# Performance work log

Hardware: AMD Instinct MI355X
Metric: run time of the kernel (lower is better)

Reference implementation:

```python
import jax, jax.numpy as jnp
import numpy as np
from jax import lax

KS = 11          # kernel_size
SIGMA = 1.5
MAX_VAL = 1.0
C1 = (0.01 * MAX_VAL) ** 2
C2 = (0.03 * MAX_VAL) ** 2
EPS = 1e-12
PAD = KS // 2    # use_padding=True -> reflect pad


def _gaussian_kernel3d():
    ax = jnp.arange(KS, dtype=jnp.float32) - (KS - 1) / 2.0
    g = jnp.exp(-(ax[:, None, None] ** 2 + ax[None, :, None] ** 2 + ax[None, None, :] ** 2)
                / (2.0 * SIGMA ** 2))
    return g / g.sum()  # (KS, KS, KS)


def setup_inputs() -> dict:
    key = jax.random.key(0)
    k1, k2 = jax.random.split(key)
    shape = (2, 1, 160, 160, 160)
    source = jax.random.uniform(k1, shape, dtype=jnp.float32)
    reference_vol = jax.random.uniform(k2, shape, dtype=jnp.float32)
    return {"source": source, "reference": reference_vol}


def reference(source, reference):
    B, C, H, W, D = source.shape
    # reflect pad spatial dims (torch 'reflect' == numpy 'reflect')
    pad_cfg = ((0, 0), (0, 0), (PAD, PAD), (PAD, PAD), (PAD, PAD))
    src = jnp.pad(source, pad_cfg, mode="reflect")
    ref = jnp.pad(reference, pad_cfg, mode="reflect")

    # fuse the 5 depthwise convolutions into one grouped conv over stacked channels
    stacked = jnp.concatenate([src, ref, src * src, ref * ref, src * ref], axis=1)  # (B,5C,...)
    kern = _gaussian_kernel3d()[None, None]                      # (1,1,KS,KS,KS)
    kern = jnp.tile(kern, (5 * C, 1, 1, 1, 1))                   # (5C,1,KS,KS,KS)
    out = lax.conv_general_dilated(
        stacked, kern, window_strides=(1, 1, 1), padding="VALID",
        feature_group_count=5 * C,
        dimension_numbers=("NCDHW", "OIDHW", "NCDHW"))           # (B,5C,H,W,D)

    mu1 = out[:, 0 * C:1 * C]
    mu2 = out[:, 1 * C:2 * C]
    m11 = out[:, 2 * C:3 * C]
    m22 = out[:, 3 * C:4 * C]
    m12 = out[:, 4 * C:5 * C]

    mu1_sq = mu1 * mu1
    mu2_sq = mu2 * mu2
    mu1_mu2 = mu1 * mu2
    sigma1_sq = m11 - mu1_sq
    sigma2_sq = m22 - mu2_sq
    sigma12 = m12 - mu1_mu2

    numerator = (2.0 * mu1_mu2 + C1) * (2.0 * sigma12 + C2)
    denominator = (mu1_sq + mu2_sq + C1) * (sigma1_sq + sigma2_sq + C2)
    ssim = numerator / (denominator + EPS)
    return 1.0 - ssim.mean()
```

## Files before the change

kernel.cpp:

```cpp
#include <hip/hip_runtime.h>
#include <math.h>

#define HH 160
#define WW 160
#define DD 160
#define VOL (HH*WW*DD)
#define KS 11
#define PAD 5
#define NBATCH 2
#define NTOT (NBATCH*VOL)
#define WCH 32
#define HCH 32

struct Wts { float w[KS]; };

__device__ __forceinline__ int mirror(int i, int n) {
    if (i < 0) i = -i;
    if (i >= n) i = 2*n - 2 - i;
    return i;
}

__global__ void init_out(float* out) {
    if (threadIdx.x == 0 && blockIdx.x == 0) out[0] = 1.0f;
}

__global__ __launch_bounds__(256) void k1(const float* __restrict__ src,
                                          const float* __restrict__ ref,
                                          float* __restrict__ B, Wts wts) {
    const int colsBlocks = HH * DD / 256;
    int colblk = blockIdx.x % colsBlocks;
    int rest   = blockIdx.x / colsBlocks;
    int wch    = rest % (WW / WCH);
    int b      = rest / (WW / WCH);
    int col    = colblk * 256 + threadIdx.x;
    int h = col / DD, d = col % DD;
    const int w0 = wch * WCH;

    const float* sp = src + (size_t)b * VOL + (size_t)h * WW * DD;
    const float* rp = ref + (size_t)b * VOL + (size_t)h * WW * DD;
    float*       op = B   + (size_t)b * 5 * VOL + (size_t)h * WW * DD + d;

    int midx[KS];
#pragma unroll
    for (int k = 0; k < KS; ++k) midx[k] = mirror(d - PAD + k, DD);

    float acc[5][KS];
#pragma unroll
    for (int c = 0; c < 5; ++c)
#pragma unroll
        for (int s = 0; s < KS; ++s) acc[c][s] = 0.f;

    const int NSTEP = WCH + 2 * PAD;
    for (int tb = 0; tb < 44; tb += 11) {
#pragma unroll
        for (int ts = 0; ts < 11; ++ts) {
            int t = tb + ts;
            if (t < NSTEP) {
                int wm   = mirror(w0 - PAD + t, WW);
                int woff = wm * DD;
                float mu1 = 0.f, mu2 = 0.f, m11 = 0.f, m22 = 0.f, m12 = 0.f;
#pragma unroll
                for (int k = 0; k < KS; ++k) {
                    float s = sp[woff + midx[k]];
                    float r = rp[woff + midx[k]];
                    float wt = wts.w[k];
                    float p = wt * s, q = wt * r;
                    mu1 += p; mu2 += q;
                    m11 = fmaf(p, s, m11);
                    m22 = fmaf(q, r, m22);
                    m12 = fmaf(p, r, m12);
                }
                float v[5] = {mu1, mu2, m11, m22, m12};
#pragma unroll
                for (int m = 0; m < 11; ++m) {
                    int slot = (ts + m) % 11;
                    float wt = wts.w[10 - m];
#pragma unroll
                    for (int c = 0; c < 5; ++c)
                        acc[c][slot] = fmaf(wt, v[c], acc[c][slot]);
                }
                int o = w0 - 10 + t;
                if (t >= 10) {
#pragma unroll
                    for (int c = 0; c < 5; ++c)
                        op[(size_t)c * VOL + (size_t)o * DD] = acc[c][ts];
                }
#pragma unroll
                for (int c = 0; c < 5; ++c) acc[c][ts] = 0.f;
            }
        }
    }
}

__global__ __launch_bounds__(256) void k2(const float* __restrict__ B,
                                          float* __restrict__ out,
                                          Wts wts, float scale) {
    const int colsBlocks = WW * DD / 256;
    int colblk = blockIdx.x % colsBlocks;
    int rest   = blockIdx.x / colsBlocks;
    int hch    = rest % (HH / HCH);
    int b      = rest / (HH / HCH);
    int col    = colblk * 256 + threadIdx.x;
    const int h0 = hch * HCH;
    const float* p = B + (size_t)b * 5 * VOL + col;
    const size_t HS = (size_t)WW * DD;

    float acc[5][KS];
#pragma unroll
    for (int c = 0; c < 5; ++c)
#pragma unroll
        for (int s = 0; s < KS; ++s) acc[c][s] = 0.f;

    float ssum = 0.f;
    const int NSTEP = HCH + 2 * PAD;
    for (int tb = 0; tb < 44; tb += 11) {
#pragma unroll
        for (int ts = 0; ts < 11; ++ts) {
            int t = tb + ts;
            if (t < NSTEP) {
                int hm = mirror(h0 - PAD + t, HH);
                size_t off = (size_t)hm * HS;
                float v0 = p[off];
                float v1 = p[off + 1 * (size_t)VOL];
                float v2 = p[off + 2 * (size_t)VOL];
                float v3 = p[off + 3 * (size_t)VOL];
                float v4 = p[off + 4 * (size_t)VOL];
#pragma unroll
                for (int m = 0; m < 11; ++m) {
                    int slot = (ts + m) % 11;
                    float wt = wts.w[10 - m];
                    acc[0][slot] = fmaf(wt, v0, acc[0][slot]);
                    acc[1][slot] = fmaf(wt, v1, acc[1][slot]);
                    acc[2][slot] = fmaf(wt, v2, acc[2][slot]);
                    acc[3][slot] = fmaf(wt, v3, acc[3][slot]);
                    acc[4][slot] = fmaf(wt, v4, acc[4][slot]);
                }
                if (t >= 10) {
                    float mu1 = acc[0][ts], mu2 = acc[1][ts];
                    float m11 = acc[2][ts], m22 = acc[3][ts], m12 = acc[4][ts];
                    float mu1sq = mu1 * mu1, mu2sq = mu2 * mu2, mu12 = mu1 * mu2;
                    float s1 = m11 - mu1sq, s2 = m22 - mu2sq, s12 = m12 - mu12;
                    const float C1 = 1e-4f, C2 = 9e-4f;
                    float num = (2.f * mu12 + C1) * (2.f * s12 + C2);
                    float den = (mu1sq + mu2sq + C1) * (s1 + s2 + C2);
                    ssum += num / (den + 1e-12f);
                }
#pragma unroll
                for (int c = 0; c < 5; ++c) acc[c][ts] = 0.f;
            }
        }
    }

#pragma unroll
    for (int off = 32; off > 0; off >>= 1)
        ssum += __shfl_down(ssum, off, 64);
    __shared__ float lsum[4];
    int lane = threadIdx.x & 63, wid = threadIdx.x >> 6;
    if (lane == 0) lsum[wid] = ssum;
    __syncthreads();
    if (threadIdx.x == 0) {
        float s = lsum[0] + lsum[1] + lsum[2] + lsum[3];
        atomicAdd(out, -s * scale);
    }
}

__global__ void brute(const float* __restrict__ src, const float* __restrict__ ref,
                      float* __restrict__ out, Wts wts, float scale) {
    long gi = (long)blockIdx.x * blockDim.x + threadIdx.x;
    float ssim = 0.f;
    if (gi < NTOT) {
        int v = (int)(gi % VOL);
        int b = (int)(gi / VOL);
        int d = v % DD;
        int w = (v / DD) % WW;
        int h = v / (DD * WW);
        const float* sp = src + (long)b * VOL;
        const float* rp = ref + (long)b * VOL;
        float a0 = 0.f, a1 = 0.f, a2 = 0.f, a3 = 0.f, a4 = 0.f;
        for (int i = 0; i < KS; ++i) {
            int hm = mirror(h + i - PAD, HH);
            float wx = wts.w[i];
            for (int j = 0; j < KS; ++j) {
                int wm = mirror(w + j - PAD, WW);
                float wxy = wx * wts.w[j];
                const float* sr = sp + ((long)hm * WW + wm) * DD;
                const float* rr = rp + ((long)hm * WW + wm) * DD;
                for (int k = 0; k < KS; ++k) {
                    int dm = mirror(d + k - PAD, DD);
                    float wt = wxy * wts.w[k];
                    float s = sr[dm], r = rr[dm];
                    a0 += wt * s; a1 += wt * r; a2 += wt * s * s;
                    a3 += wt * r * r; a4 += wt * s * r;
                }
            }
        }
        float mu1sq = a0 * a0, mu2sq = a1 * a1, mu12 = a0 * a1;
        float s1 = a2 - mu1sq, s2 = a3 - mu2sq, s12 = a4 - mu12;
        const float C1 = 1e-4f, C2 = 9e-4f;
        float num = (2.f * mu12 + C1) * (2.f * s12 + C2);
        float den = (mu1sq + mu2sq + C1) * (s1 + s2 + C2);
        ssim = num / (den + 1e-12f);
    }
#pragma unroll
    for (int off = 32; off > 0; off >>= 1)
        ssim += __shfl_down(ssim, off, 64);
    __shared__ float lsum[4];
    int lane = threadIdx.x & 63, wid = threadIdx.x >> 6;
    if (lane == 0) lsum[wid] = ssim;
    __syncthreads();
    if (threadIdx.x == 0) {
        float s = lsum[0] + lsum[1] + lsum[2] + lsum[3];
        atomicAdd(out, -s * scale);
    }
}

extern "C" void kernel_launch(void* const* d_in, const int* in_sizes, int n_in,
                              void* d_out, int out_size, void* d_ws, size_t ws_size,
                              hipStream_t stream) {
    const float* src = (const float*)d_in[0];
    const float* ref = (const float*)d_in[1];
    float* out = (float*)d_out;

    Wts wts;
    {
        double g[KS], s = 0.0;
        for (int i = 0; i < KS; ++i) {
            double a = (double)i - (KS - 1) / 2.0;
            g[i] = exp(-(a * a) / (2.0 * 1.5 * 1.5));
            s += g[i];
        }
        for (int i = 0; i < KS; ++i) wts.w[i] = (float)(g[i] / s);
    }

    const float scale = 1.0f / (float)NTOT;
    const size_t need = (size_t)NBATCH * 5 * VOL * sizeof(float);

    init_out<<<1, 64, 0, stream>>>(out);

    if (ws_size >= need) {
        float* B = (float*)d_ws;
        const int g1 = NBATCH * (WW / WCH) * (HH * DD / 256);
        const int g2 = NBATCH * (HH / HCH) * (WW * DD / 256);
        k1<<<g1, 256, 0, stream>>>(src, ref, B, wts);
        k2<<<g2, 256, 0, stream>>>(B, out, wts, scale);
    } else {
        const int BLK = 256;
        const long g = (NTOT + BLK - 1) / BLK;
        brute<<<(int)g, BLK, 0, stream>>>(src, ref, out, wts, scale);
    }
}
```

Measured before the change: 213.5 us.

## Fuse separable SSIM passes into one tiled kernel using shared-memory W convolution

Replaces the two-kernel scheme, which wrote a five-channel intermediate volume to global memory and read it back, with a single kernel. Each block owns a 16x16 (W,D) tile and streams along H. Per H-plane it convolves along D from global memory into a double-buffered LDS tile (with W halo), convolves along W from LDS, then keeps a register ring over H. This removes the large intermediate global round trip. In exchange it adds a block barrier per plane and recomputes the D-pass on halo rows (26 of 16 W rows). Loads along D are now only 16-wide, and the single __syncthreads per plane with a two-deep buffer may race between the W-pass reading buffer t&1 and the writes to the same buffer at t+2.

```diff
diff --git a/kernel.cpp b/kernel.cpp
--- a/kernel.cpp
+++ b/kernel.cpp
@@ -9,8 +9,15 @@
 #define PAD 5
 #define NBATCH 2
 #define NTOT (NBATCH*VOL)
-#define WCH 32
-#define HCH 32
+
+#define WT 16
+#define DT 16
+#define HT 32
+#define WPN (WT + 2*PAD)
+#define NP  (WPN * DT)
+#define LROW (2*DT + 2)
+#define LPLANE (WPN * LROW)
+#define LBUF (3 * LPLANE)
 
 struct Wts { float w[KS]; };
 
@@ -24,25 +31,50 @@
     if (threadIdx.x == 0 && blockIdx.x == 0) out[0] = 1.0f;
 }
 
-__global__ __launch_bounds__(256) void k1(const float* __restrict__ src,
-                                          const float* __restrict__ ref,
-                                          float* __restrict__ B, Wts wts) {
-    const int colsBlocks = HH * DD / 256;
-    int colblk = blockIdx.x % colsBlocks;
-    int rest   = blockIdx.x / colsBlocks;
-    int wch    = rest % (WW / WCH);
-    int b      = rest / (WW / WCH);
-    int col    = colblk * 256 + threadIdx.x;
-    int h = col / DD, d = col % DD;
-    const int w0 = wch * WCH;
-
-    const float* sp = src + (size_t)b * VOL + (size_t)h * WW * DD;
-    const float* rp = ref + (size_t)b * VOL + (size_t)h * WW * DD;
-    float*       op = B   + (size_t)b * 5 * VOL + (size_t)h * WW * DD + d;
-
-    int midx[KS];
-#pragma unroll
-    for (int k = 0; k < KS; ++k) midx[k] = mirror(d - PAD + k, DD);
+__global__ __launch_bounds__(256) void fused(const float* __restrict__ src,
+                                             const float* __restrict__ ref,
+                                             float* __restrict__ out,
+                                             Wts wts, float scale) {
+    __shared__ float sd[2][LBUF];
+
+    const int bx  = blockIdx.x;
+    const int dt_ = bx % (DD/DT);
+    const int wt_ = (bx / (DD/DT)) % (WW/WT);
+    const int ht_ = (bx / ((DD/DT)*(WW/WT))) % (HH/HT);
+    const int b   = bx / ((DD/DT)*(WW/WT)*(HH/HT));
+    const int d0 = dt_*DT, w0 = wt_*WT, h0 = ht_*HT;
+
+    const int tid = threadIdx.x;
+    const float* __restrict__ sp = src + (size_t)b*VOL;
+    const float* __restrict__ rp = ref + (size_t)b*VOL;
+
+    int tap0[KS], tap1[KS];
+    int ws0, ws1;
+    {
+        int wp = tid / DT, dl = tid % DT;
+        int wm = mirror(w0 - PAD + wp, WW);
+        int da = d0 + dl;
+#pragma unroll
+        for (int k = 0; k < KS; ++k)
+            tap0[k] = wm*DD + mirror(da - PAD + k, DD);
+        ws0 = wp*LROW + 2*dl;
+    }
+    const int pi1 = tid + 256;
+    const bool act1 = (pi1 < NP);
+    {
+        int pi = act1 ? pi1 : tid;
+        int wp = pi / DT, dl = pi % DT;
+        int wm = mirror(w0 - PAD + wp, WW);
+        int da = d0 + dl;
+#pragma unroll
+        for (int k = 0; k < KS; ++k)
+            tap1[k] = wm*DD + mirror(da - PAD + k, DD);
+        ws1 = wp*LROW + 2*dl;
+    }
+
+    const int wl  = tid / DT;
+    const int dl2 = tid % DT;
+    const int rb  = wl*LROW + 2*dl2;
 
     float acc[5][KS];
 #pragma unroll
@@ -50,85 +82,70 @@
 #pragma unroll
         for (int s = 0; s < KS; ++s) acc[c][s] = 0.f;
 
-    const int NSTEP = WCH + 2 * PAD;
+    float ssum = 0.f;
+    const int NSTEP = HT + 2*PAD;
+
     for (int tb = 0; tb < 44; tb += 11) {
 #pragma unroll
         for (int ts = 0; ts < 11; ++ts) {
-            int t = tb + ts;
+            const int t = tb + ts;
             if (t < NSTEP) {
-                int wm   = mirror(w0 - PAD + t, WW);
-                int woff = wm * DD;
-                float mu1 = 0.f, mu2 = 0.f, m11 = 0.f, m22 = 0.f, m12 = 0.f;
+                const int hm = mirror(h0 - PAD + t, HH);
+                const float* __restrict__ sh = sp + (size_t)hm*(WW*DD);
+                const float* __restrict__ rh = rp + (size_t)hm*(WW*DD);
+                float* __restrict__ buf = sd[t & 1];
+
+                {
+                    float mu1=0.f, mu2=0.f, m11=0.f, m22=0.f, m12=0.f;
+#pragma unroll
+                    for (int k = 0; k < KS; ++k) {
+                        float s = sh[tap0[k]];
+                        float r = rh[tap0[k]];
+                        float wt = wts.w[k];
+                        float p = wt*s, q = wt*r;
+                        mu1 += p; mu2 += q;
+                        m11 = fmaf(p, s, m11);
+                        m22 = fmaf(q, r, m22);
+                        m12 = fmaf(p, r, m12);
+                    }
+                    buf[ws0]              = mu1; buf[ws0+1]            = mu2;
+                    buf[LPLANE + ws0]     = m11; buf[LPLANE + ws0+1]   = m22;
+                    buf[2*LPLANE + ws0]   = m12;
+                }
+                if (act1) {
+                    float mu1=0.f, mu2=0.f, m11=0.f, m22=0.f, m12=0.f;
+#pragma unroll
+                    for (int k = 0; k < KS; ++k) {
+                        float s = sh[tap1[k]];
+                        float r = rh[tap1[k]];
+                        float wt = wts.w[k];
+                        float p = wt*s, q = wt*r;
+                        mu1 += p; mu2 += q;
+                        m11 = fmaf(p, s, m11);
+                        m22 = fmaf(q, r, m22);
+                        m12 = fmaf(p, r, m12);
+                    }
+                    buf[ws1]              = mu1; buf[ws1+1]            = mu2;
+                    buf[LPLANE + ws1]     = m11; buf[LPLANE + ws1+1]   = m22;
+                    buf[2*LPLANE + ws1]   = m12;
+                }
+                __syncthreads();
+
+                float v0=0.f, v1=0.f, v2=0.f, v3=0.f, v4=0.f;
 #pragma unroll
                 for (int k = 0; k < KS; ++k) {
-                    float s = sp[woff + midx[k]];
-                    float r = rp[woff + midx[k]];
-                    float wt = wts.w[k];
-                    float p = wt * s, q = wt * r;
-                    mu1 += p; mu2 += q;
-                    m11 = fmaf(p, s, m11);
-                    m22 = fmaf(q, r, m22);
-                    m12 = fmaf(p, r, m12);
-                }
-                float v[5] = {mu1, mu2, m11, m22, m12};
+                    const int o = rb + k*LROW;
+                    const float wt = wts.w[k];
+                    v0 = fmaf(wt, buf[o],              v0);
+                    v1 = fmaf(wt, buf[o+1],            v1);
+                    v2 = fmaf(wt, buf[LPLANE + o],     v2);
+                    v3 = fmaf(wt, buf[LPLANE + o+1],   v3);
+                    v4 = fmaf(wt, buf[2*LPLANE + o],   v4);
+                }
 #pragma unroll
                 for (int m = 0; m < 11; ++m) {
-                    int slot = (ts + m) % 11;
-                    float wt = wts.w[10 - m];
-#pragma unroll
-                    for (int c = 0; c < 5; ++c)
-                        acc[c][slot] = fmaf(wt, v[c], acc[c][slot]);
-                }
-                int o = w0 - 10 + t;
-                if (t >= 10) {
-#pragma unroll
-                    for (int c = 0; c < 5; ++c)
-                        op[(size_t)c * VOL + (size_t)o * DD] = acc[c][ts];
-                }
-#pragma unroll
-                for (int c = 0; c < 5; ++c) acc[c][ts] = 0.f;
-            }
-        }
-    }
-}
-
-__global__ __launch_bounds__(256) void k2(const float* __restrict__ B,
-                                          float* __restrict__ out,
-                                          Wts wts, float scale) {
-    const int colsBlocks = WW * DD / 256;
-    int colblk = blockIdx.x % colsBlocks;
-    int rest   = blockIdx.x / colsBlocks;
-    int hch    = rest % (HH / HCH);
-    int b      = rest / (HH / HCH);
-    int col    = colblk * 256 + threadIdx.x;
-    const int h0 = hch * HCH;
-    const float* p = B + (size_t)b * 5 * VOL + col;
-    const size_t HS = (size_t)WW * DD;
-
-    float acc[5][KS];
-#pragma unroll
-    for (int c = 0; c < 5; ++c)
-#pragma unroll
-        for (int s = 0; s < KS; ++s) acc[c][s] = 0.f;
-
-    float ssum = 0.f;
-    const int NSTEP = HCH + 2 * PAD;
-    for (int tb = 0; tb < 44; tb += 11) {
-#pragma unroll
-        for (int ts = 0; ts < 11; ++ts) {
-            int t = tb + ts;
-            if (t < NSTEP) {
-                int hm = mirror(h0 - PAD + t, HH);
-                size_t off = (size_t)hm * HS;
-                float v0 = p[off];
-                float v1 = p[off + 1 * (size_t)VOL];
-                float v2 = p[off + 2 * (size_t)VOL];
-                float v3 = p[off + 3 * (size_t)VOL];
-                float v4 = p[off + 4 * (size_t)VOL];
-#pragma unroll
-                for (int m = 0; m < 11; ++m) {
-                    int slot = (ts + m) % 11;
-                    float wt = wts.w[10 - m];
+                    const int slot = (ts + m) % 11;
+                    const float wt = wts.w[10 - m];
                     acc[0][slot] = fmaf(wt, v0, acc[0][slot]);
                     acc[1][slot] = fmaf(wt, v1, acc[1][slot]);
                     acc[2][slot] = fmaf(wt, v2, acc[2][slot]);
@@ -138,10 +155,10 @@
                 if (t >= 10) {
                     float mu1 = acc[0][ts], mu2 = acc[1][ts];
                     float m11 = acc[2][ts], m22 = acc[3][ts], m12 = acc[4][ts];
-                    float mu1sq = mu1 * mu1, mu2sq = mu2 * mu2, mu12 = mu1 * mu2;
+                    float mu1sq = mu1*mu1, mu2sq = mu2*mu2, mu12 = mu1*mu2;
                     float s1 = m11 - mu1sq, s2 = m22 - mu2sq, s12 = m12 - mu12;
                     const float C1 = 1e-4f, C2 = 9e-4f;
-                    float num = (2.f * mu12 + C1) * (2.f * s12 + C2);
+                    float num = (2.f*mu12 + C1) * (2.f*s12 + C2);
                     float den = (mu1sq + mu2sq + C1) * (s1 + s2 + C2);
                     ssum += num / (den + 1e-12f);
                 }
@@ -155,63 +172,11 @@
     for (int off = 32; off > 0; off >>= 1)
         ssum += __shfl_down(ssum, off, 64);
     __shared__ float lsum[4];
-    int lane = threadIdx.x & 63, wid = threadIdx.x >> 6;
+    int lane = tid & 63, wid = tid >> 6;
     if (lane == 0) lsum[wid] = ssum;
     __syncthreads();
-    if (threadIdx.x == 0) {
-        float s = lsum[0] + lsum[1] + lsum[2] + lsum[3];
-        atomicAdd(out, -s * scale);
-    }
-}
-
-__global__ void brute(const float* __restrict__ src, const float* __restrict__ ref,
-                      float* __restrict__ out, Wts wts, float scale) {
-    long gi = (long)blockIdx.x * blockDim.x + threadIdx.x;
-    float ssim = 0.f;
-    if (gi < NTOT) {
-        int v = (int)(gi % VOL);
-        int b = (int)(gi / VOL);
-        int d = v % DD;
-        int w = (v / DD) % WW;
-        int h = v / (DD * WW);
-        const float* sp = src + (long)b * VOL;
-        const float* rp = ref + (long)b * VOL;
-        float a0 = 0.f, a1 = 0.f, a2 = 0.f, a3 = 0.f, a4 = 0.f;
-        for (int i = 0; i < KS; ++i) {
-            int hm = mirror(h + i - PAD, HH);
-            float wx = wts.w[i];
-            for (int j = 0; j < KS; ++j) {
-                int wm = mirror(w + j - PAD, WW);
-                float wxy = wx * wts.w[j];
-                const float* sr = sp + ((long)hm * WW + wm) * DD;
-                const float* rr = rp + ((long)hm * WW + wm) * DD;
-                for (int k = 0; k < KS; ++k) {
-                    int dm = mirror(d + k - PAD, DD);
-                    float wt = wxy * wts.w[k];
-                    float s = sr[dm], r = rr[dm];
-                    a0 += wt * s; a1 += wt * r; a2 += wt * s * s;
-                    a3 += wt * r * r; a4 += wt * s * r;
-                }
-            }
-        }
-        float mu1sq = a0 * a0, mu2sq = a1 * a1, mu12 = a0 * a1;
-        float s1 = a2 - mu1sq, s2 = a3 - mu2sq, s12 = a4 - mu12;
-        const float C1 = 1e-4f, C2 = 9e-4f;
-        float num = (2.f * mu12 + C1) * (2.f * s12 + C2);
-        float den = (mu1sq + mu2sq + C1) * (s1 + s2 + C2);
-        ssim = num / (den + 1e-12f);
-    }
-#pragma unroll
-    for (int off = 32; off > 0; off >>= 1)
-        ssim += __shfl_down(ssim, off, 64);
-    __shared__ float lsum[4];
-    int lane = threadIdx.x & 63, wid = threadIdx.x >> 6;
-    if (lane == 0) lsum[wid] = ssim;
-    __syncthreads();
-    if (threadIdx.x == 0) {
-        float s = lsum[0] + lsum[1] + lsum[2] + lsum[3];
-        atomicAdd(out, -s * scale);
-    }
+    if (tid == 0)
+        atomicAdd(out, -(lsum[0]+lsum[1]+lsum[2]+lsum[3]) * scale);
 }
 
 extern "C" void kernel_launch(void* const* d_in, const int* in_sizes, int n_in,
@@ -233,19 +198,8 @@
     }
 
     const float scale = 1.0f / (float)NTOT;
-    const size_t need = (size_t)NBATCH * 5 * VOL * sizeof(float);
 
     init_out<<<1, 64, 0, stream>>>(out);
-
-    if (ws_size >= need) {
-        float* B = (float*)d_ws;
-        const int g1 = NBATCH * (WW / WCH) * (HH * DD / 256);
-        const int g2 = NBATCH * (HH / HCH) * (WW * DD / 256);
-        k1<<<g1, 256, 0, stream>>>(src, ref, B, wts);
-        k2<<<g2, 256, 0, stream>>>(B, out, wts, scale);
-    } else {
-        const int BLK = 256;
-        const long g = (NTOT + BLK - 1) / BLK;
-        brute<<<(int)g, BLK, 0, stream>>>(src, ref, out, wts, scale);
-    }
-}
+    const int g = NBATCH * (HH/HT) * (WW/WT) * (DD/DT);
+    fused<<<g, 256, 0, stream>>>(src, ref, out, wts, scale);
+}
```

Result: slower. 223.1 us (+4.5%).
